# Performance work log

Hardware: AMD Instinct MI355X
Metric: run time of the kernel (lower is better)

## Reference

```python
import jax, jax.numpy as jnp
import numpy as np

MAX_TOP_K = 64          # max(top_k) across the batch, as in sample_from_logit dispatch
NEG_INF = -1e30
B, V, T = 256, 128000, 16


def setup_inputs() -> dict:
    key = jax.random.key(0)
    k1, k2, k3, k4, k5, k6 = jax.random.split(key, 6)
    logits = jax.random.normal(k1, (B, V), dtype=jnp.float32)
    temperature = jax.random.uniform(k2, (B,), dtype=jnp.float32) + 0.5   # (0.5, 1.5)
    top_k = jax.random.randint(k3, (B,), 1, MAX_TOP_K, dtype=jnp.int32)
    top_p = jax.random.uniform(k4, (B,), dtype=jnp.float32)               # (0, 1)
    min_p = jax.random.uniform(k5, (B,), dtype=jnp.float32) * 0.1         # small min-p
    target_ids = jax.random.randint(k6, (B, T), 0, V, dtype=jnp.int32)
    return {"logits": logits, "temperature": temperature, "top_k": top_k,
            "top_p": top_p, "min_p": min_p, "target_ids": target_ids}


def _sample_from_logit(logits, temperature, top_k, top_p, min_p):
    # temperature scaling
    temp = jnp.maximum(temperature, 0.05)
    scaled = logits / temp[:, None]                    # [B, V]
    # restrict to the max_top_k candidates once (sorted descending)
    vals, idx = jax.lax.top_k(scaled, MAX_TOP_K)       # [B, K], [B, K]
    pos = jnp.arange(MAX_TOP_K)[None, :]
    k = jnp.clip(top_k, 1, MAX_TOP_K)
    keep_k = pos < k[:, None]                          # per-request top-k mask
    vals = jnp.where(keep_k, vals, NEG_INF)
    probs = jax.nn.softmax(vals, axis=-1)              # renormalized over kept set
    # top-p (nucleus): keep tokens whose preceding cumulative mass < top_p
    csum = jnp.cumsum(probs, axis=-1)
    keep_p = (csum - probs) < top_p[:, None]
    # min-p: keep tokens with prob >= min_p * max_prob (max is column 0, sorted desc)
    keep_m = probs >= min_p[:, None] * probs[:, :1]
    keep = (keep_k & keep_p & keep_m).at[:, 0].set(True)  # always keep the argmax
    filt_logp = jnp.where(keep, jnp.log(probs + 1e-20), NEG_INF)
    # multinomial sample via Gumbel-max (renormalization is implicit)
    g = jax.random.gumbel(jax.random.key(42), filt_logp.shape, dtype=filt_logp.dtype)
    choice = jnp.argmax(filt_logp + g, axis=-1)        # [B] index into top-K set
    return jnp.take_along_axis(idx, choice[:, None], axis=1)[:, 0]  # vocab ids


def reference(logits, temperature, top_k, top_p, min_p, target_ids):
    next_token_ids = _sample_from_logit(logits, temperature, top_k, top_p, min_p)  # [B]
    # perplexity gather: ppls = -log_softmax(logits); ppl[i, j] = ppls[i, target_ids[i, j]]
    logZ = jax.nn.logsumexp(logits, axis=-1, keepdims=True)          # [B, 1]
    tgt_logits = jnp.take_along_axis(logits, target_ids, axis=1)     # [B, T]
    ppl = -(tgt_logits - logZ)                                       # [B, T]
    return next_token_ids, ppl
```

## Files before the change

kernel.cpp:

```cpp
#include <hip/hip_runtime.h>
#include <stdint.h>

typedef unsigned long long ull;

#define B_ 256
#define V_ 128000
#define T_ 16
#define K_ 64
#define NEG_INF_ (-1e30f)

#define CAP   4096
#define NT    1024
#define PER   8

__device__ __forceinline__ uint32_t rotl32(uint32_t x, uint32_t d) {
  return (x << d) | (x >> (32u - d));
}

__device__ uint32_t threefry_bits_partitionable(uint32_t f) {
  const uint32_t ks0 = 0u;
  const uint32_t ks1 = 42u;
  const uint32_t ks2 = 0x1BD11BDAu ^ 0u ^ 42u;
  uint32_t x0 = 0u;
  uint32_t x1 = f;
  x0 += ks0; x1 += ks1;
#define R4(a,b,c,d) \
  x0 += x1; x1 = rotl32(x1,a); x1 ^= x0; \
  x0 += x1; x1 = rotl32(x1,b); x1 ^= x0; \
  x0 += x1; x1 = rotl32(x1,c); x1 ^= x0; \
  x0 += x1; x1 = rotl32(x1,d); x1 ^= x0;
  R4(13u,15u,26u,6u)   x0 += ks1; x1 += ks2 + 1u;
  R4(17u,29u,16u,24u)  x0 += ks2; x1 += ks0 + 2u;
  R4(13u,15u,26u,6u)   x0 += ks0; x1 += ks1 + 3u;
  R4(17u,29u,16u,24u)  x0 += ks1; x1 += ks2 + 4u;
  R4(13u,15u,26u,6u)   x0 += ks2; x1 += ks0 + 5u;
#undef R4
  return x0 ^ x1;
}

__global__ __launch_bounds__(NT) void sampler_kernel(
    const float* __restrict__ logits,
    const float* __restrict__ temperature,
    const int*   __restrict__ top_k,
    const float* __restrict__ top_p,
    const float* __restrict__ min_p,
    const int*   __restrict__ target_ids,
    float*       __restrict__ out)
{
  const int r   = blockIdx.x;
  const int tid = threadIdx.x;
  const float* __restrict__ row = logits + (size_t)r * V_;

  __shared__ ull          s_cand[CAP];
  __shared__ unsigned int s_candcount;
  __shared__ float        s_wavesum[NT / 64];
  __shared__ ull          s_top[K_];
  __shared__ float        s_g[K_];
  __shared__ float        s_e[K_];
  __shared__ float        s_pi[K_];
  __shared__ float        s_lg[K_];
  __shared__ float        s_logZ, s_sum;
  __shared__ int          s_ncand;

  if (tid < K_) s_top[tid] = 0ull;
  if (tid == 0) s_candcount = 0u;
  __syncthreads();

  const float temp = fmaxf(temperature[r], 0.05f);

  float a0 = 0.0f, a1 = 0.0f, a2 = 0.0f, a3 = 0.0f;
  const float4* row4 = reinterpret_cast<const float4*>(row);
  const int nf4 = V_ / 4;
  const int STRIDE = NT * PER;

#define SUMEXP(b) do {                                                         \
    a0 += __expf((b).x); a1 += __expf((b).y);                                  \
    a2 += __expf((b).z); a3 += __expf((b).w);                                  \
  } while (0)

#define HARVEST(b, i4) do {                                                    \
    float xs_[4] = {(b).x, (b).y, (b).z, (b).w};                               \
    _Pragma("unroll")                                                          \
    for (int c_ = 0; c_ < 4; ++c_) {                                           \
      if (xs_[c_] > 3.0f) {                                                    \
        unsigned int slot_ = atomicAdd(&s_candcount, 1u);                      \
        if (slot_ < CAP) {                                                     \
          float scaled_ = xs_[c_] / temp;                                      \
          uint32_t idx_ = (uint32_t)((i4) * 4 + c_);                           \
          s_cand[slot_] = ((ull)__float_as_uint(scaled_) << 32) |              \
                          (ull)(0xFFFFFFFFu - idx_);                           \
        }                                                                      \
      }                                                                        \
    }                                                                          \
  } while (0)

  int base = 0;
  for (; base + STRIDE <= nf4; base += STRIDE) {
    float4 b[PER];
#pragma unroll
    for (int j = 0; j < PER; ++j) b[j] = row4[base + tid + j * NT];
    float mx = NEG_INF_;
#pragma unroll
    for (int j = 0; j < PER; ++j)
      mx = fmaxf(mx, fmaxf(fmaxf(b[j].x, b[j].y), fmaxf(b[j].z, b[j].w)));
#pragma unroll
    for (int j = 0; j < PER; ++j) SUMEXP(b[j]);
    if (mx > 3.0f) {
#pragma unroll
      for (int j = 0; j < PER; ++j) HARVEST(b[j], base + tid + j * NT);
    }
  }
  {
    float4 b[PER];
    int    ix[PER];
#pragma unroll
    for (int j = 0; j < PER; ++j) {
      ix[j] = base + tid + j * NT;
      b[j] = make_float4(NEG_INF_, NEG_INF_, NEG_INF_, NEG_INF_);
      if (ix[j] < nf4) b[j] = row4[ix[j]];
    }
    float mx = NEG_INF_;
#pragma unroll
    for (int j = 0; j < PER; ++j)
      mx = fmaxf(mx, fmaxf(fmaxf(b[j].x, b[j].y), fmaxf(b[j].z, b[j].w)));
#pragma unroll
    for (int j = 0; j < PER; ++j) SUMEXP(b[j]);
    if (mx > 3.0f) {
#pragma unroll
      for (int j = 0; j < PER; ++j) HARVEST(b[j], ix[j]);
    }
  }
#undef SUMEXP
#undef HARVEST

  float esum = (a0 + a1) + (a2 + a3);
  for (int off = 32; off > 0; off >>= 1) esum += __shfl_down(esum, off, 64);
  if ((tid & 63) == 0) s_wavesum[tid >> 6] = esum;
  __syncthreads();
  if (tid == 0) {
    float t = 0.0f;
    for (int w = 0; w < NT / 64; ++w) t += s_wavesum[w];
    s_logZ = logf(t);
    int nc = (int)s_candcount; if (nc > CAP) nc = CAP;
    s_ncand = nc;
  }
  __syncthreads();

  int ncand = s_ncand;
  for (int tier = 0; tier < 2 && ncand < K_; ++tier) {
    if (tid == 0) s_candcount = 0u;
    __syncthreads();
    const float thr = (tier == 0) ? 2.0f : -3.0e38f;
    for (int i = tid; i < V_; i += NT) {
      float x = row[i];
      if (x >= thr) {
        unsigned int slot = atomicAdd(&s_candcount, 1u);
        if (slot < CAP) {
          float scaled = x / temp;
          s_cand[slot] = ((ull)__float_as_uint(scaled) << 32) |
                         (ull)(0xFFFFFFFFu - (uint32_t)i);
        }
      }
    }
    __syncthreads();
    if (tid == 0) { int nc = (int)s_candcount; if (nc > CAP) nc = CAP; s_ncand = nc; }
    __syncthreads();
    ncand = s_ncand;
  }

  if (tid < K_) {
    uint32_t bits = threefry_bits_partitionable((uint32_t)(r * K_ + tid));
    float u01 = __uint_as_float((bits >> 9) | 0x3f800000u) - 1.0f;
    const float tiny = 1.1754943508222875e-38f;
    float u = fmaxf(tiny, u01 * (1.0f - tiny) + tiny);
    s_g[tid] = -logf(-logf(u));
  }

  if (tid < T_) {
    int tgt = target_ids[r * T_ + tid];
    out[B_ + r * T_ + tid] = s_logZ - row[tgt];
  }

  for (int c = tid; c < ncand; c += NT) {
    ull key = s_cand[c];
    int rank = 0;
    for (int j = 0; j < ncand; ++j) rank += (s_cand[j] > key) ? 1 : 0;
    if (rank < K_) s_top[rank] = key;
  }
  __syncthreads();

  const int kk_raw = top_k[r];
  const int kk = kk_raw < 1 ? 1 : (kk_raw > K_ ? K_ : kk_raw);
  const int nn = ncand < K_ ? ncand : K_;

  if (tid < K_) {
    float v = (tid < nn) ? __uint_as_float((uint32_t)(s_top[tid] >> 32)) : NEG_INF_;
    if (tid >= kk) v = NEG_INF_;
    float v0 = (0 < nn) ? __uint_as_float((uint32_t)(s_top[0] >> 32)) : NEG_INF_;
    s_e[tid] = expf(v - v0);
  }
  __syncthreads();
  if (tid == 0) {
    float sum = 0.0f;
    for (int i = 0; i < K_; ++i) sum += s_e[i];
    s_sum = sum;
  }
  __syncthreads();
  if (tid < K_) {
    float pi = s_e[tid] / s_sum;
    s_pi[tid] = pi;
    s_lg[tid] = logf(pi + 1e-20f);
  }
  __syncthreads();
  if (tid == 0) {
    const float tp = top_p[r], mp = min_p[r];
    const float p0 = s_pi[0];
    float csum = 0.0f, best = -INFINITY;
    int choice = 0;
    for (int i = 0; i < K_; ++i) {
      float pi = s_pi[i];
      csum += pi;
      bool keep = (i < kk) && ((csum - pi) < tp) && (pi >= mp * p0);
      if (i == 0) keep = true;
      float fl = keep ? s_lg[i] : NEG_INF_;
      float sc = fl + s_g[i];
      if (sc > best) { best = sc; choice = i; }
    }
    int token = (int)(0xFFFFFFFFu - (uint32_t)(s_top[choice] & 0xFFFFFFFFull));
    out[r] = (float)token;
  }
}

extern "C" void kernel_launch(void* const* d_in, const int* in_sizes, int n_in,
                              void* d_out, int out_size, void* d_ws, size_t ws_size,
                              hipStream_t stream) {
  const float* logits      = (const float*)d_in[0];
  const float* temperature = (const float*)d_in[1];
  const int*   top_k       = (const int*)d_in[2];
  const float* top_p       = (const float*)d_in[3];
  const float* min_p       = (const float*)d_in[4];
  const int*   target_ids  = (const int*)d_in[5];
  float* out = (float*)d_out;
  (void)in_sizes; (void)n_in; (void)out_size; (void)d_ws; (void)ws_size;

  hipLaunchKernelGGL(sampler_kernel, dim3(B_), dim3(NT), 0, stream,
                     logits, temperature, top_k, top_p, min_p, target_ids, out);
}
```

Baseline: 37.77 us.

## Software-pipeline the row streaming loop and hoist Gumbel/target work before it

```diff
diff --git a/kernel.cpp b/kernel.cpp
--- a/kernel.cpp
+++ b/kernel.cpp
@@ -9,9 +9,12 @@
 #define K_ 64
 #define NEG_INF_ (-1e30f)
 
-#define CAP   4096
-#define NT    1024
-#define PER   8
+#define CAP    4096
+#define NT     1024
+#define PER    4
+#define STRIDE (NT * PER)
+#define NF4    (V_ / 4)
+#define NBURST ((NF4 + STRIDE - 1) / STRIDE)
 
 __device__ __forceinline__ uint32_t rotl32(uint32_t x, uint32_t d) {
   return (x << d) | (x >> (32u - d));
@@ -56,82 +59,88 @@
   __shared__ float        s_wavesum[NT / 64];
   __shared__ ull          s_top[K_];
   __shared__ float        s_g[K_];
+  __shared__ float        s_tgt[T_];
   __shared__ float        s_e[K_];
   __shared__ float        s_pi[K_];
   __shared__ float        s_lg[K_];
   __shared__ float        s_logZ, s_sum;
   __shared__ int          s_ncand;
 
-  if (tid < K_) s_top[tid] = 0ull;
   if (tid == 0) s_candcount = 0u;
+
+  if (tid < K_) {
+    uint32_t bits = threefry_bits_partitionable((uint32_t)(r * K_ + tid));
+    float u01 = __uint_as_float((bits >> 9) | 0x3f800000u) - 1.0f;
+    const float tiny = 1.1754943508222875e-38f;
+    float u = fmaxf(tiny, u01 * (1.0f - tiny) + tiny);
+    s_g[tid] = -logf(-logf(u));
+  }
+  if (tid >= 64 && tid < 64 + T_) {
+    int i = tid - 64;
+    int tgt = target_ids[r * T_ + i];
+    s_tgt[i] = row[tgt];
+  }
+  if (tid >= 128 && tid < 128 + K_) s_top[tid - 128] = 0ull;
   __syncthreads();
 
   const float temp = fmaxf(temperature[r], 0.05f);
 
   float a0 = 0.0f, a1 = 0.0f, a2 = 0.0f, a3 = 0.0f;
   const float4* row4 = reinterpret_cast<const float4*>(row);
-  const int nf4 = V_ / 4;
-  const int STRIDE = NT * PER;
 
 #define SUMEXP(b) do {                                                         \
     a0 += __expf((b).x); a1 += __expf((b).y);                                  \
     a2 += __expf((b).z); a3 += __expf((b).w);                                  \
   } while (0)
 
-#define HARVEST(b, i4) do {                                                    \
-    float xs_[4] = {(b).x, (b).y, (b).z, (b).w};                               \
-    _Pragma("unroll")                                                          \
-    for (int c_ = 0; c_ < 4; ++c_) {                                           \
-      if (xs_[c_] > 3.0f) {                                                    \
-        unsigned int slot_ = atomicAdd(&s_candcount, 1u);                      \
-        if (slot_ < CAP) {                                                     \
-          float scaled_ = xs_[c_] / temp;                                      \
-          uint32_t idx_ = (uint32_t)((i4) * 4 + c_);                           \
-          s_cand[slot_] = ((ull)__float_as_uint(scaled_) << 32) |              \
-                          (ull)(0xFFFFFFFFu - idx_);                           \
+#define GPROC(b, i4) do {                                                      \
+    SUMEXP(b);                                                                 \
+    float m4_ = fmaxf(fmaxf((b).x, (b).y), fmaxf((b).z, (b).w));               \
+    if (m4_ > 3.0f) {                                                          \
+      float xs_[4] = {(b).x, (b).y, (b).z, (b).w};                             \
+      _Pragma("unroll")                                                        \
+      for (int c_ = 0; c_ < 4; ++c_) {                                         \
+        if (xs_[c_] > 3.0f) {                                                  \
+          unsigned int slot_ = atomicAdd(&s_candcount, 1u);                    \
+          if (slot_ < CAP) {                                                   \
+            float scaled_ = xs_[c_] / temp;                                    \
+            uint32_t idx_ = (uint32_t)((i4) * 4 + c_);                         \
+            s_cand[slot_] = ((ull)__float_as_uint(scaled_) << 32) |            \
+                            (ull)(0xFFFFFFFFu - idx_);                         \
+          }                                                                    \
         }                                                                      \
       }                                                                        \
     }                                                                          \
   } while (0)
 
-  int base = 0;
-  for (; base + STRIDE <= nf4; base += STRIDE) {
-    float4 b[PER];
-#pragma unroll
-    for (int j = 0; j < PER; ++j) b[j] = row4[base + tid + j * NT];
-    float mx = NEG_INF_;
-#pragma unroll
-    for (int j = 0; j < PER; ++j)
-      mx = fmaxf(mx, fmaxf(fmaxf(b[j].x, b[j].y), fmaxf(b[j].z, b[j].w)));
-#pragma unroll
-    for (int j = 0; j < PER; ++j) SUMEXP(b[j]);
-    if (mx > 3.0f) {
-#pragma unroll
-      for (int j = 0; j < PER; ++j) HARVEST(b[j], base + tid + j * NT);
+  {
+    float4 cur[PER], nxt[PER];
+#pragma unroll
+    for (int j = 0; j < PER; ++j) cur[j] = row4[tid + j * NT];
+#pragma unroll
+    for (int bu = 0; bu < NBURST; ++bu) {
+      const int cbase = bu * STRIDE;
+      if (bu + 1 < NBURST) {
+        const int nbase = cbase + STRIDE;
+#pragma unroll
+        for (int j = 0; j < PER; ++j) {
+          const int ix = nbase + tid + j * NT;
+          if (nbase + (j + 1) * NT <= NF4) {
+            nxt[j] = row4[ix];
+          } else {
+            nxt[j] = (ix < NF4) ? row4[ix]
+                   : make_float4(NEG_INF_, NEG_INF_, NEG_INF_, NEG_INF_);
+          }
+        }
+      }
+#pragma unroll
+      for (int j = 0; j < PER; ++j) GPROC(cur[j], cbase + tid + j * NT);
+#pragma unroll
+      for (int j = 0; j < PER; ++j) cur[j] = nxt[j];
     }
   }
-  {
-    float4 b[PER];
-    int    ix[PER];
-#pragma unroll
-    for (int j = 0; j < PER; ++j) {
-      ix[j] = base + tid + j * NT;
-      b[j] = make_float4(NEG_INF_, NEG_INF_, NEG_INF_, NEG_INF_);
-      if (ix[j] < nf4) b[j] = row4[ix[j]];
-    }
-    float mx = NEG_INF_;
-#pragma unroll
-    for (int j = 0; j < PER; ++j)
-      mx = fmaxf(mx, fmaxf(fmaxf(b[j].x, b[j].y), fmaxf(b[j].z, b[j].w)));
-#pragma unroll
-    for (int j = 0; j < PER; ++j) SUMEXP(b[j]);
-    if (mx > 3.0f) {
-#pragma unroll
-      for (int j = 0; j < PER; ++j) HARVEST(b[j], ix[j]);
-    }
-  }
+#undef GPROC
 #undef SUMEXP
-#undef HARVEST
 
   float esum = (a0 + a1) + (a2 + a3);
   for (int off = 32; off > 0; off >>= 1) esum += __shfl_down(esum, off, 64);
@@ -145,6 +154,8 @@
     s_ncand = nc;
   }
   __syncthreads();
+
+  if (tid < T_) out[B_ + r * T_ + tid] = s_logZ - s_tgt[tid];
 
   int ncand = s_ncand;
   for (int tier = 0; tier < 2 && ncand < K_; ++tier) {
@@ -168,19 +179,6 @@
     ncand = s_ncand;
   }
 
-  if (tid < K_) {
-    uint32_t bits = threefry_bits_partitionable((uint32_t)(r * K_ + tid));
-    float u01 = __uint_as_float((bits >> 9) | 0x3f800000u) - 1.0f;
-    const float tiny = 1.1754943508222875e-38f;
-    float u = fmaxf(tiny, u01 * (1.0f - tiny) + tiny);
-    s_g[tid] = -logf(-logf(u));
-  }
-
-  if (tid < T_) {
-    int tgt = target_ids[r * T_ + tid];
-    out[B_ + r * T_ + tid] = s_logZ - row[tgt];
-  }
-
   for (int c = tid; c < ncand; c += NT) {
     ull key = s_cand[c];
     int rank = 0;
```

Result: slower. 42.23 us (+11.8%).
